# Kernel optimization log

Hardware: AMD Instinct MI355X
Metric: run time of the kernel (lower is better)

The kernel has to match this reference:

```python
import jax, jax.numpy as jnp
import numpy as np

NW = 16        # nwindows
NEUR = 128     # neurons per layer
NHID = 2       # hidden-1 square layers (hidden=3)
N = 65536      # collocation points
SIGMA = 0.02   # window sharpness
DOM = (0.0, 1.0)
OVERLAP = 0.25
U_MEAN = 0.0
U_SD = 1.0


def _partition():
    width = (DOM[1] - DOM[0]) / NW
    sub = np.zeros((NW, 2), np.float32)
    for i in range(NW):
        sub[i, 0] = DOM[0] if i == 0 else DOM[0] + (i - OVERLAP / 2) * width
        sub[i, 1] = DOM[1] if i == NW - 1 else DOM[0] + (i + 1 + OVERLAP / 2) * width
    means = (sub[:, 0] + sub[:, 1]) / 2
    std = (sub[:, 1] - sub[:, 0]) / 2
    mids = np.zeros(NW + 1, np.float32)
    mids[0] = sub[0, 0]
    mids[-1] = sub[-1, 1]
    mids[1:-1] = (sub[:-1, 1] + sub[1:, 0]) / 2
    return means.astype(np.float32), std.astype(np.float32), mids


def setup_inputs() -> dict:
    key = jax.random.key(0)
    ks = jax.random.split(key, 7)
    means, std, mids = _partition()
    x = jax.random.uniform(ks[0], (N, 1), jnp.float32)  # points in [0,1) = domain
    W_in = jax.random.normal(ks[1], (NW, 1, NEUR), jnp.float32)            # fan_in=1
    b_in = 0.1 * jax.random.normal(ks[2], (NW, NEUR), jnp.float32)
    W_hid = jax.random.normal(ks[3], (NHID, NW, NEUR, NEUR), jnp.float32) / np.sqrt(NEUR)
    b_hid = 0.1 * jax.random.normal(ks[4], (NHID, NW, NEUR), jnp.float32)
    W_out = jax.random.normal(ks[5], (NW, NEUR, 1), jnp.float32) / np.sqrt(NEUR)
    b_out = 0.1 * jax.random.normal(ks[6], (NW, 1), jnp.float32)
    return {"x": x, "means": jnp.asarray(means), "std": jnp.asarray(std),
            "mids": jnp.asarray(mids), "W_in": W_in, "b_in": b_in,
            "W_hid": W_hid, "b_hid": b_hid, "W_out": W_out, "b_out": b_out}


def reference(x, means, std, mids, W_in, b_in, W_hid, b_hid, W_out, b_out):
    # Grouped over all windows at once (torch code loops over windows).
    # x: [N,1] -> x_norm: [W,N,1]
    x_norm = (x[None, :, :] - means[:, None, None]) / std[:, None, None]
    h = jnp.tanh(jnp.einsum('wni,wio->wno', x_norm, W_in) + b_in[:, None, :])  # [W,N,NEUR]
    for l in range(NHID):  # fixed small structural loop
        h = jnp.tanh(jnp.einsum('wnd,wde->wne', h, W_hid[l]) + b_hid[l][:, None, :])
    out = jnp.einsum('wnd,wdo->wno', h, W_out) + b_out[:, None, :]  # [W,N,1]
    out = out * U_SD + U_MEAN
    # window fn exactly as torch: 1/(1+exp(x_left)) * 1/(1+exp(-x_right))
    x_left = (x[None, :, :] - mids[:-1, None, None]) / SIGMA
    x_right = (x[None, :, :] - mids[1:, None, None]) / SIGMA
    window = jax.nn.sigmoid(-x_left) * jax.nn.sigmoid(x_right)  # [W,N,1]
    return jnp.sum(window * out, axis=0)  # [N,1]
```

## Files before the change

### kernel.cpp

```cpp
#include <hip/hip_runtime.h>

#define NW    16
#define NEUR  128
#define NPTS  65536
#define SIGMA 0.02f
#define U_MEAN 0.0f
#define U_SD   1.0f
#define DELTA 0.19f

#define TILE   128
#define NTHR   512
#define HPAD   136
#define WMAT_HALVES (NEUR*HPAD)
#define WT_TOTAL (2*NW*WMAT_HALVES)
#define WT_BYTES (WT_TOTAL*2)
#define CNT_OFF  WT_BYTES
#define IDX_OFF  (WT_BYTES + 1024)
#define NSEG   16
#define SEGPTS (NPTS/NSEG)
#define CAPSEG 2048
#define CHUNKS 256

typedef _Float16 half8 __attribute__((ext_vector_type(8)));
typedef float    f32x4 __attribute__((ext_vector_type(4)));

__device__ __forceinline__ float tanh_fast(float x) {
    float e = __expf(2.0f * x);
    return 1.0f - 2.0f * __builtin_amdgcn_rcpf(1.0f + e);
}

__global__ __launch_bounds__(512) void aux_kernel(
    const float* __restrict__ W_hid, const float* __restrict__ x,
    const float* __restrict__ mids,  _Float16* __restrict__ wt,
    int* __restrict__ cnt16, unsigned short* __restrict__ idx,
    float* __restrict__ out)
{
    const int b = blockIdx.x;
    const int t = threadIdx.x;

    if (b < 32) {
        __shared__ __align__(16) _Float16 tile[NEUR * HPAD];
        const int lw = b;
        const float4* src = (const float4*)(W_hid + (size_t)lw * NEUR * NEUR);
#pragma unroll
        for (int it = 0; it < 8; ++it) {
            int f4 = it * 512 + t;
            int d  = f4 >> 5;
            int e0 = (f4 & 31) << 2;
            float4 v = src[f4];
            tile[(e0 + 0) * HPAD + d] = (_Float16)v.x;
            tile[(e0 + 1) * HPAD + d] = (_Float16)v.y;
            tile[(e0 + 2) * HPAD + d] = (_Float16)v.z;
            tile[(e0 + 3) * HPAD + d] = (_Float16)v.w;
        }
        if (t < NEUR) {
            half8 z; for (int j = 0; j < 8; ++j) z[j] = (_Float16)0.0f;
            *(half8*)&tile[t * HPAD + NEUR] = z;
        }
        __syncthreads();
        _Float16* dst = wt + (size_t)lw * WMAT_HALVES;
#pragma unroll
        for (int it = 0; it < 5; ++it) {
            int chunk = it * 512 + t;
            if (chunk < WMAT_HALVES / 8)
                *(half8*)&dst[chunk * 8] = *(const half8*)&tile[chunk * 8];
        }
    } else if (b < 288) {
        const int s = (b - 32) & (NSEG - 1);
        const int w = (b - 32) >> 4;
        __shared__ int lcnt;
        if (t == 0) lcnt = 0;
        __syncthreads();
        const float lo = mids[w] - DELTA;
        const float hi = mids[w + 1] + DELTA;
        const int lane = t & 63;
        unsigned short* dst = idx + (size_t)(w * NSEG + s) * CAPSEG;
#pragma unroll
        for (int it = 0; it < SEGPTS / 512; ++it) {
            int i = s * SEGPTS + it * 512 + t;
            float xv = x[i];
            bool need = (xv >= lo) && (xv <= hi);
            unsigned long long mask = __ballot(need);
            if (mask) {
                int leader = (int)__builtin_ctzll(mask);
                int total  = (int)__popcll(mask);
                int rank   = (int)__popcll(mask & ((1ull << lane) - 1ull));
                int base = 0;
                if (lane == leader) base = atomicAdd(&lcnt, total);
                base = __shfl(base, leader);
                int slot = base + rank;
                if (need && slot < CAPSEG) dst[slot] = (unsigned short)i;
            }
        }
        __syncthreads();
        if (t == 0) cnt16[w * NSEG + s] = lcnt;
    } else {
        int i4 = (b - 288) * 512 + t;
        float4 z = {0.f, 0.f, 0.f, 0.f};
        ((float4*)out)[i4] = z;
    }
}

__device__ __forceinline__ void gemm_tile(const _Float16* Abase, const _Float16* Bbase,
                                          int row0, int m, int q, f32x4 acc[8]) {
#pragma unroll
    for (int s = 0; s < 4; ++s) {
        half8 a = *(const half8*)(Abase + (row0 + m) * HPAD + s * 32 + q * 8);
#pragma unroll
        for (int c = 0; c < 8; ++c) {
            half8 b = *(const half8*)(Bbase + (c * 16 + m) * HPAD + s * 32 + q * 8);
            acc[c] = __builtin_amdgcn_mfma_f32_16x16x32_f16(a, b, acc[c], 0, 0, 0);
        }
    }
}

__device__ __forceinline__ void act_store(_Float16* Hbase, const float* __restrict__ bias,
                                          int row0, int m, int q, const f32x4 acc[8]) {
#pragma unroll
    for (int c = 0; c < 8; ++c) {
        float b = bias[c * 16 + m];
#pragma unroll
        for (int r = 0; r < 4; ++r) {
            Hbase[(row0 + q * 4 + r) * HPAD + c * 16 + m] = (_Float16)tanh_fast(acc[c][r] + b);
        }
    }
}

__device__ __forceinline__ void stage_w(const float4* __restrict__ g, float4* l4, int t) {
    float4 r0 = g[t], r1 = g[t + 512], r2 = g[t + 1024], r3 = g[t + 1536];
    float4 r4;
    if (t < 128) r4 = g[t + 2048];
    l4[t] = r0; l4[t + 512] = r1; l4[t + 1024] = r2; l4[t + 1536] = r3;
    if (t < 128) l4[t + 2048] = r4;
}

__global__ __launch_bounds__(NTHR, 4) void fbpinn_main(
    const float* __restrict__ x,     const float* __restrict__ means,
    const float* __restrict__ stds,  const float* __restrict__ mids,
    const float* __restrict__ W_in,  const float* __restrict__ b_in,
    const float* __restrict__ b_hid, const float* __restrict__ W_out,
    const float* __restrict__ b_out, const _Float16* __restrict__ wt,
    const int* __restrict__ cnt16,   const unsigned short* __restrict__ idx,
    float* __restrict__ out)
{
    const int w    = blockIdx.y;
    const int base = blockIdx.x * TILE;

    __shared__ __align__(16) _Float16 WA[WMAT_HALVES];
    __shared__ __align__(16) _Float16 WB[WMAT_HALVES];
    __shared__ float xs[TILE];
    __shared__ float wouts[NEUR];
    __shared__ unsigned short gis[TILE];

    const int t    = threadIdx.x;
    const int lane = t & 63;
    const int wave = t >> 6;
    const int m    = lane & 15;
    const int q    = lane >> 4;
    const int row0 = wave * 16;
    const int rsel = m & 3;

    int csh[NSEG];
    int total = 0;
#pragma unroll
    for (int k = 0; k < NSEG; ++k) {
        int c = cnt16[w * NSEG + k];
        c = c > CAPSEG ? CAPSEG : c;
        csh[k] = c;
        total += c;
    }
    if (base >= total) return;
    const int nvalid = min(TILE, total - base);

    if (t < TILE) {
        int v = base + min(t, nvalid - 1);
        int seg = 0, segbase = 0, pre = 0;
#pragma unroll
        for (int k = 0; k < NSEG - 1; ++k) {
            pre += csh[k];
            if (v >= pre) { seg = k + 1; segbase = pre; }
        }
        unsigned short gi = idx[(size_t)(w * NSEG + seg) * CAPSEG + (v - segbase)];
        gis[t] = gi;
        xs[t]  = x[gi];
    }
    stage_w((const float4*)(wt + (size_t)(0 * NW + w) * WMAT_HALVES), (float4*)WA, t);
    stage_w((const float4*)(wt + (size_t)(1 * NW + w) * WMAT_HALVES), (float4*)WB, t);
    if (t < NEUR) wouts[t] = W_out[w * NEUR + t];
    __syncthreads();

    const float xn = (xs[row0 + m] - means[w]) * __builtin_amdgcn_rcpf(stds[w]);
    const float* win = W_in + w * NEUR;
    const float* bin = b_in + w * NEUR;
    half8 af[4];
#pragma unroll
    for (int s = 0; s < 4; ++s) {
        const int n0 = s * 32 + q * 8;
        float4 wv0 = *(const float4*)&win[n0];
        float4 wv1 = *(const float4*)&win[n0 + 4];
        float4 bv0 = *(const float4*)&bin[n0];
        float4 bv1 = *(const float4*)&bin[n0 + 4];
        af[s][0] = (_Float16)tanh_fast(fmaf(xn, wv0.x, bv0.x));
        af[s][1] = (_Float16)tanh_fast(fmaf(xn, wv0.y, bv0.y));
        af[s][2] = (_Float16)tanh_fast(fmaf(xn, wv0.z, bv0.z));
        af[s][3] = (_Float16)tanh_fast(fmaf(xn, wv0.w, bv0.w));
        af[s][4] = (_Float16)tanh_fast(fmaf(xn, wv1.x, bv1.x));
        af[s][5] = (_Float16)tanh_fast(fmaf(xn, wv1.y, bv1.y));
        af[s][6] = (_Float16)tanh_fast(fmaf(xn, wv1.z, bv1.z));
        af[s][7] = (_Float16)tanh_fast(fmaf(xn, wv1.w, bv1.w));
    }

    f32x4 acc[8];
    const f32x4 zz = {0.f, 0.f, 0.f, 0.f};
#pragma unroll
    for (int c = 0; c < 8; ++c) acc[c] = zz;
#pragma unroll
    for (int s = 0; s < 4; ++s) {
#pragma unroll
        for (int c = 0; c < 8; ++c) {
            half8 b = *(const half8*)(WA + (c * 16 + m) * HPAD + s * 32 + q * 8);
            acc[c] = __builtin_amdgcn_mfma_f32_16x16x32_f16(af[s], b, acc[c], 0, 0, 0);
        }
    }
    __syncthreads();

    act_store(WA, b_hid + (0 * NW + w) * NEUR, row0, m, q, acc);
    __syncthreads();

#pragma unroll
    for (int c = 0; c < 8; ++c) acc[c] = zz;
    gemm_tile(WA, WB, row0, m, q, acc);

    const float* bh1 = b_hid + (1 * NW + w) * NEUR;
    float t0 = 0.f, t1 = 0.f, t2 = 0.f, t3 = 0.f;
#pragma unroll
    for (int c = 0; c < 8; ++c) {
        float b  = bh1[c * 16 + m];
        float wo = wouts[c * 16 + m];
        t0 = fmaf(tanh_fast(acc[c][0] + b), wo, t0);
        t1 = fmaf(tanh_fast(acc[c][1] + b), wo, t1);
        t2 = fmaf(tanh_fast(acc[c][2] + b), wo, t2);
        t3 = fmaf(tanh_fast(acc[c][3] + b), wo, t3);
    }
    t0 += __shfl_xor(t0, 1); t1 += __shfl_xor(t1, 1);
    t2 += __shfl_xor(t2, 1); t3 += __shfl_xor(t3, 1);
    t0 += __shfl_xor(t0, 2); t1 += __shfl_xor(t1, 2);
    t2 += __shfl_xor(t2, 2); t3 += __shfl_xor(t3, 2);
    float v = (rsel == 0) ? t0 : (rsel == 1) ? t1 : (rsel == 2) ? t2 : t3;
    v += __shfl_xor(v, 4);
    v += __shfl_xor(v, 8);

    const int slot = row0 + q * 4 + rsel;
    if (m < 4 && slot < nvalid) {
        float u   = (v + b_out[w]) * U_SD + U_MEAN;
        float xv  = xs[slot];
        float xl  = (xv - mids[w])     * (1.0f / SIGMA);
        float xr  = (xv - mids[w + 1]) * (1.0f / SIGMA);
        float wf  = __builtin_amdgcn_rcpf(1.0f + __expf(xl)) *
                    __builtin_amdgcn_rcpf(1.0f + __expf(-xr));
        atomicAdd(&out[gis[slot]], wf * u);
    }
}

extern "C" void kernel_launch(void* const* d_in, const int* in_sizes, int n_in,
                              void* d_out, int out_size, void* d_ws, size_t ws_size,
                              hipStream_t stream) {
    const float* x     = (const float*)d_in[0];
    const float* means = (const float*)d_in[1];
    const float* stds  = (const float*)d_in[2];
    const float* mids  = (const float*)d_in[3];
    const float* W_in  = (const float*)d_in[4];
    const float* b_in  = (const float*)d_in[5];
    const float* W_hid = (const float*)d_in[6];
    const float* b_hid = (const float*)d_in[7];
    const float* W_out = (const float*)d_in[8];
    const float* b_out = (const float*)d_in[9];
    float* out = (float*)d_out;

    _Float16*       wt    = (_Float16*)d_ws;
    int*            cnt16 = (int*)((char*)d_ws + CNT_OFF);
    unsigned short* idx   = (unsigned short*)((char*)d_ws + IDX_OFF);

    aux_kernel<<<320, 512, 0, stream>>>(W_hid, x, mids, wt, cnt16, idx, out);
    fbpinn_main<<<dim3(CHUNKS, NW), NTHR, 0, stream>>>(
        x, means, stds, mids, W_in, b_in, b_hid, W_out, b_out, wt, cnt16, idx, out);
}
```

Measured before the change: 158.1 us.

## Pre-swizzle hidden weights into MFMA fragment order and load directly from global

The aux kernel now writes each hidden weight matrix in per-lane MFMA B-fragment order, so the main kernel reads B operands straight from global/L2 with coalesced 16-byte loads instead of staging two full matrices in LDS. LDS use drops to a single activation buffer, which allows raising the launch bound to 8 blocks per SM and removes two block-wide barriers, since each wave only touches its own activation rows. The trade-off is more global/L2 traffic per block, with MFMA operands now fetched repeatedly from cache rather than from LDS.

After: 169.4 us. 7.2% more time.

```diff
diff --git a/kernel.cpp b/kernel.cpp
--- a/kernel.cpp
+++ b/kernel.cpp
@@ -11,9 +11,9 @@
 #define TILE   128
 #define NTHR   512
 #define HPAD   136
-#define WMAT_HALVES (NEUR*HPAD)
-#define WT_TOTAL (2*NW*WMAT_HALVES)
-#define WT_BYTES (WT_TOTAL*2)
+#define MAT_HALVES 16384
+#define WT_HALVES (2*NW*MAT_HALVES)
+#define WT_BYTES (WT_HALVES*2)
 #define CNT_OFF  WT_BYTES
 #define IDX_OFF  (WT_BYTES + 1024)
 #define NSEG   16
@@ -53,17 +53,16 @@
             tile[(e0 + 2) * HPAD + d] = (_Float16)v.z;
             tile[(e0 + 3) * HPAD + d] = (_Float16)v.w;
         }
-        if (t < NEUR) {
-            half8 z; for (int j = 0; j < 8; ++j) z[j] = (_Float16)0.0f;
-            *(half8*)&tile[t * HPAD + NEUR] = z;
-        }
         __syncthreads();
-        _Float16* dst = wt + (size_t)lw * WMAT_HALVES;
-#pragma unroll
-        for (int it = 0; it < 5; ++it) {
-            int chunk = it * 512 + t;
-            if (chunk < WMAT_HALVES / 8)
-                *(half8*)&dst[chunk * 8] = *(const half8*)&tile[chunk * 8];
+        half8* dst8 = (half8*)(wt + (size_t)lw * MAT_HALVES);
+#pragma unroll
+        for (int it = 0; it < 4; ++it) {
+            int h8 = it * 512 + t;
+            int sc = h8 >> 6;
+            int ln = h8 & 63;
+            int s_ = sc >> 3, c_ = sc & 7;
+            int q_ = ln >> 4, m_ = ln & 15;
+            dst8[h8] = *(const half8*)&tile[(c_ * 16 + m_) * HPAD + s_ * 32 + q_ * 8];
         }
     } else if (b < 288) {
         const int s = (b - 32) & (NSEG - 1);
@@ -101,40 +100,7 @@
     }
 }
 
-__device__ __forceinline__ void gemm_tile(const _Float16* Abase, const _Float16* Bbase,
-                                          int row0, int m, int q, f32x4 acc[8]) {
-#pragma unroll
-    for (int s = 0; s < 4; ++s) {
-        half8 a = *(const half8*)(Abase + (row0 + m) * HPAD + s * 32 + q * 8);
-#pragma unroll
-        for (int c = 0; c < 8; ++c) {
-            half8 b = *(const half8*)(Bbase + (c * 16 + m) * HPAD + s * 32 + q * 8);
-            acc[c] = __builtin_amdgcn_mfma_f32_16x16x32_f16(a, b, acc[c], 0, 0, 0);
-        }
-    }
-}
-
-__device__ __forceinline__ void act_store(_Float16* Hbase, const float* __restrict__ bias,
-                                          int row0, int m, int q, const f32x4 acc[8]) {
-#pragma unroll
-    for (int c = 0; c < 8; ++c) {
-        float b = bias[c * 16 + m];
-#pragma unroll
-        for (int r = 0; r < 4; ++r) {
-            Hbase[(row0 + q * 4 + r) * HPAD + c * 16 + m] = (_Float16)tanh_fast(acc[c][r] + b);
-        }
-    }
-}
-
-__device__ __forceinline__ void stage_w(const float4* __restrict__ g, float4* l4, int t) {
-    float4 r0 = g[t], r1 = g[t + 512], r2 = g[t + 1024], r3 = g[t + 1536];
-    float4 r4;
-    if (t < 128) r4 = g[t + 2048];
-    l4[t] = r0; l4[t + 512] = r1; l4[t + 1024] = r2; l4[t + 1536] = r3;
-    if (t < 128) l4[t + 2048] = r4;
-}
-
-__global__ __launch_bounds__(NTHR, 4) void fbpinn_main(
+__global__ __launch_bounds__(NTHR, 8) void fbpinn_main(
     const float* __restrict__ x,     const float* __restrict__ means,
     const float* __restrict__ stds,  const float* __restrict__ mids,
     const float* __restrict__ W_in,  const float* __restrict__ b_in,
@@ -146,8 +112,7 @@
     const int w    = blockIdx.y;
     const int base = blockIdx.x * TILE;
 
-    __shared__ __align__(16) _Float16 WA[WMAT_HALVES];
-    __shared__ __align__(16) _Float16 WB[WMAT_HALVES];
+    __shared__ __align__(16) _Float16 Hlds[TILE * HPAD];
     __shared__ float xs[TILE];
     __shared__ float wouts[NEUR];
     __shared__ unsigned short gis[TILE];
@@ -184,10 +149,11 @@
         gis[t] = gi;
         xs[t]  = x[gi];
     }
-    stage_w((const float4*)(wt + (size_t)(0 * NW + w) * WMAT_HALVES), (float4*)WA, t);
-    stage_w((const float4*)(wt + (size_t)(1 * NW + w) * WMAT_HALVES), (float4*)WB, t);
     if (t < NEUR) wouts[t] = W_out[w * NEUR + t];
     __syncthreads();
+
+    const half8* b0 = (const half8*)(wt + (size_t)(0 * NW + w) * MAT_HALVES) + lane;
+    const half8* b1 = (const half8*)(wt + (size_t)(1 * NW + w) * MAT_HALVES) + lane;
 
     const float xn = (xs[row0 + m] - means[w]) * __builtin_amdgcn_rcpf(stds[w]);
     const float* win = W_in + w * NEUR;
@@ -217,19 +183,30 @@
 #pragma unroll
     for (int s = 0; s < 4; ++s) {
 #pragma unroll
+        for (int c = 0; c < 8; ++c)
+            acc[c] = __builtin_amdgcn_mfma_f32_16x16x32_f16(af[s], b0[(s * 8 + c) * 64], acc[c], 0, 0, 0);
+    }
+
+    {
+        const float* bh0 = b_hid + (0 * NW + w) * NEUR;
+#pragma unroll
         for (int c = 0; c < 8; ++c) {
-            half8 b = *(const half8*)(WA + (c * 16 + m) * HPAD + s * 32 + q * 8);
-            acc[c] = __builtin_amdgcn_mfma_f32_16x16x32_f16(af[s], b, acc[c], 0, 0, 0);
-        }
-    }
-    __syncthreads();
-
-    act_store(WA, b_hid + (0 * NW + w) * NEUR, row0, m, q, acc);
-    __syncthreads();
+            float bb = bh0[c * 16 + m];
+#pragma unroll
+            for (int r = 0; r < 4; ++r)
+                Hlds[(row0 + q * 4 + r) * HPAD + c * 16 + m] = (_Float16)tanh_fast(acc[c][r] + bb);
+        }
+    }
 
 #pragma unroll
     for (int c = 0; c < 8; ++c) acc[c] = zz;
-    gemm_tile(WA, WB, row0, m, q, acc);
+#pragma unroll
+    for (int s = 0; s < 4; ++s) {
+        half8 a = *(const half8*)(Hlds + (row0 + m) * HPAD + s * 32 + q * 8);
+#pragma unroll
+        for (int c = 0; c < 8; ++c)
+            acc[c] = __builtin_amdgcn_mfma_f32_16x16x32_f16(a, b1[(s * 8 + c) * 64], acc[c], 0, 0, 0);
+    }
 
     const float* bh1 = b_hid + (1 * NW + w) * NEUR;
     float t0 = 0.f, t1 = 0.f, t2 = 0.f, t3 = 0.f;
```

## Process two 16-row slabs per wave to reuse weight fragments across MFMAs

Applied to the files above, without the earlier changes.

The block shrinks from 512 to 256 threads, and each wave now owns 32 point rows instead of 16. Every weight fragment loaded from LDS feeds two MFMA accumulator sets, which halves LDS reads of the weight matrices per point. Because each wave only reads back the rows it wrote itself, the barrier between the hidden-activation store and the second GEMM is dropped. The cost is fewer resident waves per CU and roughly double the accumulator registers per thread, which could hurt latency hiding.

New measurement: 162.6 us. 2.8% more time.

```diff
diff --git a/kernel.cpp b/kernel.cpp
--- a/kernel.cpp
+++ b/kernel.cpp
@@ -9,7 +9,7 @@
 #define DELTA 0.19f
 
 #define TILE   128
-#define NTHR   512
+#define NTHR   256
 #define HPAD   136
 #define WMAT_HALVES (NEUR*HPAD)
 #define WT_TOTAL (2*NW*WMAT_HALVES)
@@ -101,40 +101,13 @@
     }
 }
 
-__device__ __forceinline__ void gemm_tile(const _Float16* Abase, const _Float16* Bbase,
-                                          int row0, int m, int q, f32x4 acc[8]) {
-#pragma unroll
-    for (int s = 0; s < 4; ++s) {
-        half8 a = *(const half8*)(Abase + (row0 + m) * HPAD + s * 32 + q * 8);
-#pragma unroll
-        for (int c = 0; c < 8; ++c) {
-            half8 b = *(const half8*)(Bbase + (c * 16 + m) * HPAD + s * 32 + q * 8);
-            acc[c] = __builtin_amdgcn_mfma_f32_16x16x32_f16(a, b, acc[c], 0, 0, 0);
-        }
-    }
-}
-
-__device__ __forceinline__ void act_store(_Float16* Hbase, const float* __restrict__ bias,
-                                          int row0, int m, int q, const f32x4 acc[8]) {
-#pragma unroll
-    for (int c = 0; c < 8; ++c) {
-        float b = bias[c * 16 + m];
-#pragma unroll
-        for (int r = 0; r < 4; ++r) {
-            Hbase[(row0 + q * 4 + r) * HPAD + c * 16 + m] = (_Float16)tanh_fast(acc[c][r] + b);
-        }
-    }
-}
-
 __device__ __forceinline__ void stage_w(const float4* __restrict__ g, float4* l4, int t) {
-    float4 r0 = g[t], r1 = g[t + 512], r2 = g[t + 1024], r3 = g[t + 1536];
-    float4 r4;
-    if (t < 128) r4 = g[t + 2048];
-    l4[t] = r0; l4[t + 512] = r1; l4[t + 1024] = r2; l4[t + 1536] = r3;
-    if (t < 128) l4[t + 2048] = r4;
-}
-
-__global__ __launch_bounds__(NTHR, 4) void fbpinn_main(
+#pragma unroll
+    for (int i = 0; i < 8; ++i) l4[i * 256 + t] = g[i * 256 + t];
+    if (t < 128) l4[2048 + t] = g[2048 + t];
+}
+
+__global__ __launch_bounds__(NTHR, 2) void fbpinn_main(
     const float* __restrict__ x,     const float* __restrict__ means,
     const float* __restrict__ stds,  const float* __restrict__ mids,
     const float* __restrict__ W_in,  const float* __restrict__ b_in,
@@ -157,7 +130,7 @@
     const int wave = t >> 6;
     const int m    = lane & 15;
     const int q    = lane >> 4;
-    const int row0 = wave * 16;
+    const int row0 = wave * 32;
     const int rsel = m & 3;
 
     int csh[NSEG];
@@ -189,10 +162,12 @@
     if (t < NEUR) wouts[t] = W_out[w * NEUR + t];
     __syncthreads();
 
-    const float xn = (xs[row0 + m] - means[w]) * __builtin_amdgcn_rcpf(stds[w]);
+    const float rstd = __builtin_amdgcn_rcpf(stds[w]);
+    const float xn0 = (xs[row0 + m]      - means[w]) * rstd;
+    const float xn1 = (xs[row0 + 16 + m] - means[w]) * rstd;
     const float* win = W_in + w * NEUR;
     const float* bin = b_in + w * NEUR;
-    half8 af[4];
+    half8 af0[4], af1[4];
 #pragma unroll
     for (int s = 0; s < 4; ++s) {
         const int n0 = s * 32 + q * 8;
@@ -200,65 +175,94 @@
         float4 wv1 = *(const float4*)&win[n0 + 4];
         float4 bv0 = *(const float4*)&bin[n0];
         float4 bv1 = *(const float4*)&bin[n0 + 4];
-        af[s][0] = (_Float16)tanh_fast(fmaf(xn, wv0.x, bv0.x));
-        af[s][1] = (_Float16)tanh_fast(fmaf(xn, wv0.y, bv0.y));
-        af[s][2] = (_Float16)tanh_fast(fmaf(xn, wv0.z, bv0.z));
-        af[s][3] = (_Float16)tanh_fast(fmaf(xn, wv0.w, bv0.w));
-        af[s][4] = (_Float16)tanh_fast(fmaf(xn, wv1.x, bv1.x));
-        af[s][5] = (_Float16)tanh_fast(fmaf(xn, wv1.y, bv1.y));
-        af[s][6] = (_Float16)tanh_fast(fmaf(xn, wv1.z, bv1.z));
-        af[s][7] = (_Float16)tanh_fast(fmaf(xn, wv1.w, bv1.w));
-    }
-
-    f32x4 acc[8];
+#pragma unroll
+        for (int j = 0; j < 4; ++j) {
+            float wj = ((const float*)&wv0)[j], bj = ((const float*)&bv0)[j];
+            af0[s][j] = (_Float16)tanh_fast(fmaf(xn0, wj, bj));
+            af1[s][j] = (_Float16)tanh_fast(fmaf(xn1, wj, bj));
+        }
+#pragma unroll
+        for (int j = 0; j < 4; ++j) {
+            float wj = ((const float*)&wv1)[j], bj = ((const float*)&bv1)[j];
+            af0[s][4 + j] = (_Float16)tanh_fast(fmaf(xn0, wj, bj));
+            af1[s][4 + j] = (_Float16)tanh_fast(fmaf(xn1, wj, bj));
+        }
+    }
+
+    f32x4 acc0[8], acc1[8];
     const f32x4 zz = {0.f, 0.f, 0.f, 0.f};
 #pragma unroll
-    for (int c = 0; c < 8; ++c) acc[c] = zz;
+    for (int c = 0; c < 8; ++c) { acc0[c] = zz; acc1[c] = zz; }
 #pragma unroll
     for (int s = 0; s < 4; ++s) {
 #pragma unroll
         for (int c = 0; c < 8; ++c) {
             half8 b = *(const half8*)(WA + (c * 16 + m) * HPAD + s * 32 + q * 8);
-            acc[c] = __builtin_amdgcn_mfma_f32_16x16x32_f16(af[s], b, acc[c], 0, 0, 0);
+            acc0[c] = __builtin_amdgcn_mfma_f32_16x16x32_f16(af0[s], b, acc0[c], 0, 0, 0);
+            acc1[c] = __builtin_amdgcn_mfma_f32_16x16x32_f16(af1[s], b, acc1[c], 0, 0, 0);
         }
     }
     __syncthreads();
 
-    act_store(WA, b_hid + (0 * NW + w) * NEUR, row0, m, q, acc);
-    __syncthreads();
-
-#pragma unroll
-    for (int c = 0; c < 8; ++c) acc[c] = zz;
-    gemm_tile(WA, WB, row0, m, q, acc);
+    {
+        const float* bh0 = b_hid + (0 * NW + w) * NEUR;
+#pragma unroll
+        for (int c = 0; c < 8; ++c) {
+            float bb = bh0[c * 16 + m];
+#pragma unroll
+            for (int r = 0; r < 4; ++r) {
+                WA[(row0 + q * 4 + r) * HPAD + c * 16 + m]      = (_Float16)tanh_fast(acc0[c][r] + bb);
+                WA[(row0 + 16 + q * 4 + r) * HPAD + c * 16 + m] = (_Float16)tanh_fast(acc1[c][r] + bb);
+            }
+        }
+    }
+
+#pragma unroll
+    for (int c = 0; c < 8; ++c) { acc0[c] = zz; acc1[c] = zz; }
+#pragma unroll
+    for (int s = 0; s < 4; ++s) {
+        half8 a0 = *(const half8*)(WA + (row0 + m) * HPAD + s * 32 + q * 8);
+        half8 a1 = *(const half8*)(WA + (row0 + 16 + m) * HPAD + s * 32 + q * 8);
+#pragma unroll
+        for (int c = 0; c < 8; ++c) {
+            half8 b = *(const half8*)(WB + (c * 16 + m) * HPAD + s * 32 + q * 8);
+            acc0[c] = __builtin_amdgcn_mfma_f32_16x16x32_f16(a0, b, acc0[c], 0, 0, 0);
+            acc1[c] = __builtin_amdgcn_mfma_f32_16x16x32_f16(a1, b, acc1[c], 0, 0, 0);
+        }
+    }
 
     const float* bh1 = b_hid + (1 * NW + w) * NEUR;
-    float t0 = 0.f, t1 = 0.f, t2 = 0.f, t3 = 0.f;
-#pragma unroll
-    for (int c = 0; c < 8; ++c) {
-        float b  = bh1[c * 16 + m];
-        float wo = wouts[c * 16 + m];
-        t0 = fmaf(tanh_fast(acc[c][0] + b), wo, t0);
-        t1 = fmaf(tanh_fast(acc[c][1] + b), wo, t1);
-        t2 = fmaf(tanh_fast(acc[c][2] + b), wo, t2);
-        t3 = fmaf(tanh_fast(acc[c][3] + b), wo, t3);
-    }
-    t0 += __shfl_xor(t0, 1); t1 += __shfl_xor(t1, 1);
-    t2 += __shfl_xor(t2, 1); t3 += __shfl_xor(t3, 1);
-    t0 += __shfl_xor(t0, 2); t1 += __shfl_xor(t1, 2);
-    t2 += __shfl_xor(t2, 2); t3 += __shfl_xor(t3, 2);
-    float v = (rsel == 0) ? t0 : (rsel == 1) ? t1 : (rsel == 2) ? t2 : t3;
-    v += __shfl_xor(v, 4);
-    v += __shfl_xor(v, 8);
-
-    const int slot = row0 + q * 4 + rsel;
-    if (m < 4 && slot < nvalid) {
-        float u   = (v + b_out[w]) * U_SD + U_MEAN;
-        float xv  = xs[slot];
-        float xl  = (xv - mids[w])     * (1.0f / SIGMA);
-        float xr  = (xv - mids[w + 1]) * (1.0f / SIGMA);
-        float wf  = __builtin_amdgcn_rcpf(1.0f + __expf(xl)) *
-                    __builtin_amdgcn_rcpf(1.0f + __expf(-xr));
-        atomicAdd(&out[gis[slot]], wf * u);
+#pragma unroll
+    for (int slab = 0; slab < 2; ++slab) {
+        const f32x4* acc = slab ? acc1 : acc0;
+        float t0 = 0.f, t1 = 0.f, t2 = 0.f, t3 = 0.f;
+#pragma unroll
+        for (int c = 0; c < 8; ++c) {
+            float b  = bh1[c * 16 + m];
+            float wo = wouts[c * 16 + m];
+            t0 = fmaf(tanh_fast(acc[c][0] + b), wo, t0);
+            t1 = fmaf(tanh_fast(acc[c][1] + b), wo, t1);
+            t2 = fmaf(tanh_fast(acc[c][2] + b), wo, t2);
+            t3 = fmaf(tanh_fast(acc[c][3] + b), wo, t3);
+        }
+        t0 += __shfl_xor(t0, 1); t1 += __shfl_xor(t1, 1);
+        t2 += __shfl_xor(t2, 1); t3 += __shfl_xor(t3, 1);
+        t0 += __shfl_xor(t0, 2); t1 += __shfl_xor(t1, 2);
+        t2 += __shfl_xor(t2, 2); t3 += __shfl_xor(t3, 2);
+        float v = (rsel == 0) ? t0 : (rsel == 1) ? t1 : (rsel == 2) ? t2 : t3;
+        v += __shfl_xor(v, 4);
+        v += __shfl_xor(v, 8);
+
+        const int slot = row0 + slab * 16 + q * 4 + rsel;
+        if (m < 4 && slot < nvalid) {
+            float u   = (v + b_out[w]) * U_SD + U_MEAN;
+            float xv  = xs[slot];
+            float xl  = (xv - mids[w])     * (1.0f / SIGMA);
+            float xr  = (xv - mids[w + 1]) * (1.0f / SIGMA);
+            float wf  = __builtin_amdgcn_rcpf(1.0f + __expf(xl)) *
+                        __builtin_amdgcn_rcpf(1.0f + __expf(-xr));
+            atomicAdd(&out[gis[slot]], wf * u);
+        }
     }
 }
 
```
